# Optimization experiments

Measured on AMD Instinct MI355X. Metric: run time of the kernel, lower is better.

## Reference

```python
import jax, jax.numpy as jnp
import numpy as np

POOL = 7          # pool_size
RES = 42          # ROIS_resolution
CH = 2048         # backbone output channels (Xception)
GCN_DIM = 256     # gcn_outfeat_dim (== gat_outfeat_dim after head split, heads=1)
HEADS = 1
GAT_CH = 256
ALPHA = 0.1       # APPNP teleport
EPS = 1e-3        # keras BatchNormalization epsilon
CHUNKS = CH // GCN_DIM            # 8 channel chunks per ROI
CNODES = CHUNKS * POOL * POOL     # 392 intra-graph nodes


def _rois():
    # fixed ROI boxes (x, y, w, h) on the 42x42 upsampled map:
    # 3x3 grid of 14x14 cells + two horizontal halves + full image
    c = RES // 3
    r = [(x * c, y * c, c, c) for y in range(3) for x in range(3)]
    r += [(0, 0, RES, RES // 2), (0, RES // 2, RES, RES // 2), (0, 0, RES, RES)]
    return r

ROIS = _rois()
NUM_ROIS = len(ROIS)  # 12


def _gcn_adj(n):
    # spektral GCNConv.preprocess on all-ones adjacency: D^-1/2 (A + I) D^-1/2
    a = np.ones((n, n), np.float32) + np.eye(n, dtype=np.float32)
    d = a.sum(1)
    return jnp.asarray(a / np.sqrt(np.outer(d, d)))

A_INTRA = _gcn_adj(CNODES)        # (392, 392)
A_INTER = _gcn_adj(NUM_ROIS + 1)  # (13, 13)


def _appnp(x, a, w, b):
    # APPNPConv, propagations=1, sigmoid MLP: (1-a)*A@m + a*m
    m = jax.nn.sigmoid(x @ w + b)
    return (1.0 - ALPHA) * jnp.einsum('nm,...mf->...nf', a, m) + ALPHA * m


def _gat(x, a, k, a_self, a_neigh, b):
    # GATConv._call_dense (inference: dropout off); a has add_self_loops folded in
    xp = jnp.einsum('...ni,iho->...nho', x, k)          # (...,N,H,C)
    s = jnp.einsum('...nhi,iho->...nho', xp, a_self)    # (...,N,H,1)
    t = jnp.einsum('...nhi,iho->...nho', xp, a_neigh)   # (...,N,H,1)
    coef = s + jnp.swapaxes(t, -3, -1)                  # (...,N,H,N)
    coef = jax.nn.leaky_relu(coef, 0.2)
    mask = jnp.where(a == 0.0, -1e10, 0.0)              # (N,N) (all-connected here)
    coef = jax.nn.softmax(coef + mask[:, None, :], axis=-1)
    out = jnp.einsum('...nhm,...mhi->...nhi', coef, xp)
    out = out.reshape(out.shape[:-2] + (HEADS * GAT_CH,))  # concat heads
    return jax.nn.elu(out + b)


def _gnn_block(x, a, aw, ab, gk, gs, gn, gb):
    h = _appnp(x, a, aw, ab) + x
    return _gat(h, a, gk, gs, gn, gb) + h


def setup_inputs() -> dict:
    key = jax.random.key(0)
    ks = jax.random.split(key, 8)
    s = 0.05
    return {
        'base_out': jax.random.normal(ks[0], (8, POOL, POOL, CH), jnp.float32),
        'appnp_w': jax.random.normal(ks[1], (GCN_DIM, GCN_DIM), jnp.float32) * s,
        'appnp_b': jnp.zeros((GCN_DIM,), jnp.float32),
        'gat_kernel': jax.random.normal(ks[2], (GCN_DIM, HEADS, GAT_CH), jnp.float32) * s,
        'gat_attn_self': jax.random.normal(ks[3], (GAT_CH, HEADS, 1), jnp.float32) * s,
        'gat_attn_neighs': jax.random.normal(ks[4], (GAT_CH, HEADS, 1), jnp.float32) * s,
        'gat_bias': jnp.zeros((HEADS * GAT_CH,), jnp.float32),
        'pool_feat_w': jax.random.normal(ks[5], (GCN_DIM, 2 * GCN_DIM), jnp.float32) * s,
        'pool_feat_b': jnp.zeros((2 * GCN_DIM,), jnp.float32),
        'pool_attn_w': jax.random.normal(ks[6], (GCN_DIM, 2 * GCN_DIM), jnp.float32) * s,
        'pool_attn_b': jnp.zeros((2 * GCN_DIM,), jnp.float32),
        'bn_gamma': jnp.ones((2 * GCN_DIM,), jnp.float32),
        'bn_beta': jnp.zeros((2 * GCN_DIM,), jnp.float32),
        'bn_mean': jnp.zeros((2 * GCN_DIM,), jnp.float32),
        'bn_var': jnp.ones((2 * GCN_DIM,), jnp.float32),
        'dense_w': jax.random.normal(ks[7], (2 * GCN_DIM, 200), jnp.float32) * s,
        'dense_b': jnp.zeros((200,), jnp.float32),
    }


def reference(base_out, appnp_w, appnp_b, gat_kernel, gat_attn_self, gat_attn_neighs,
              gat_bias, pool_feat_w, pool_feat_b, pool_attn_w, pool_attn_b,
              bn_gamma, bn_beta, bn_mean, bn_var, dense_w, dense_b):
    B = base_out.shape[0]
    # upsample backbone features to ROI resolution
    x0 = jax.image.resize(base_out, (B, RES, RES, CH), 'bilinear')
    # RoiPoolingConv: crop each static ROI and resize to (POOL, POOL)
    pooled = [jax.image.resize(x0[:, y:y + h, x:x + w, :], (B, POOL, POOL, CH), 'bilinear')
              for (x, y, w, h) in ROIS]
    pooled.append(base_out)  # global node (pool_size == base_out spatial dim)
    rois = jnp.stack(pooled, axis=1)  # (B, R+1, 7, 7, CH)
    # _temp_nodes_transform: split channels into CHUNKS, concat along node axis
    nodes = rois.reshape(B, NUM_ROIS + 1, POOL * POOL, CHUNKS, GCN_DIM)
    nodes = nodes.transpose(0, 1, 3, 2, 4).reshape(B, NUM_ROIS + 1, CNODES, GCN_DIM)
    gnn = (appnp_w, appnp_b, gat_kernel, gat_attn_self, gat_attn_neighs, gat_bias)
    # intra-ROI graphs: 13 independent 392-node graphs (batched over (B, R+1))
    x2_intra = _gnn_block(nodes, A_INTRA, *gnn).reshape(B, (NUM_ROIS + 1) * CNODES, GCN_DIM)
    # inter-ROI graphs: 392 independent 13-node graphs
    xt = nodes.transpose(0, 2, 1, 3)  # (B, CNODES, R+1, GCN_DIM)
    x2_inter = _gnn_block(xt, A_INTER, *gnn).reshape(B, CNODES * (NUM_ROIS + 1), GCN_DIM)
    x2 = jnp.concatenate([x2_intra, x2_inter], axis=1)  # (B, 10192, 256)
    # GlobalAttentionPool(512)
    feat = x2 @ pool_feat_w + pool_feat_b
    gate = jax.nn.sigmoid(x2 @ pool_attn_w + pool_attn_b)
    xf = jnp.sum(gate * feat, axis=1)  # (B, 512)
    # BatchNorm (inference) + softmax classifier
    xn = (xf - bn_mean) / jnp.sqrt(bn_var + EPS) * bn_gamma + bn_beta
    return jax.nn.softmax(xn @ dense_w + dense_b, axis=-1)
```

## Files before the change

### kernel.cpp

```cpp
#include <hip/hip_runtime.h>
#include <math.h>


typedef __attribute__((ext_vector_type(8))) short bf16x8;
typedef __attribute__((ext_vector_type(4))) float f32x4;
typedef __attribute__((ext_vector_type(4))) short short4v;

#define MFMA16x32(a, b, c) __builtin_amdgcn_mfma_f32_16x16x32_bf16((a), (b), (c), 0, 0, 0)

__device__ __forceinline__ float sigmoidf_(float x) { return 1.0f / (1.0f + expf(-x)); }
__device__ __forceinline__ float leakyf_(float x) { return x >= 0.0f ? x : 0.2f * x; }
__device__ __forceinline__ float eluf_(float x) { return x > 0.0f ? x : expm1f(x); }
__device__ __forceinline__ short f2bf(float f) {
  unsigned u = __builtin_bit_cast(unsigned, f);
  unsigned r = u + 0x7fffu + ((u >> 16) & 1u);
  return (short)(r >> 16);
}
__device__ __forceinline__ float bf2f(short s) {
  unsigned u = ((unsigned)(unsigned short)s) << 16;
  return __builtin_bit_cast(float, u);
}
__device__ __forceinline__ f32x4 fzero4() {
  f32x4 z;
  #pragma unroll
  for (int i = 0; i < 4; ++i) z[i] = 0.0f;
  return z;
}

__global__ void wtab_k(float* __restrict__ wtab) {
  const int RX[12] = {0,14,28, 0,14,28, 0,14,28, 0, 0, 0};
  const int RY[12] = {0, 0, 0,14,14,14,28,28,28, 0,21, 0};
  const int RW[12] = {14,14,14,14,14,14,14,14,14,42,42,42};
  const int RH[12] = {14,14,14,14,14,14,14,14,14,21,21,42};
  for (int e = threadIdx.x; e < 13 * 2 * 49; e += blockDim.x) {
    const int roi = e / 98;
    const int rest = e % 98;
    const int axis = rest / 49;
    const int o = (rest % 49) / 7;
    const int ib = rest % 7;
    float wout;
    if (roi == 12) {
      wout = (o == ib) ? 1.0f : 0.0f;
    } else {
      const int start = axis ? RX[roi] : RY[roi];
      const int len = axis ? RW[roi] : RH[roi];
      const float s = (float)len / 7.0f;
      const float oc = (o + 0.5f) * s - 0.5f;
      float wsum = 0.0f, dot = 0.0f;
      for (int j = 0; j < len; ++j) {
        float w = 1.0f - fabsf((float)j - oc) / s;
        if (w <= 0.0f) continue;
        wsum += w;
        const float ic = ((float)(start + j) + 0.5f) / 6.0f - 0.5f;
        const float fl = floorf(ic);
        const int ia = (int)fl;
        const float fr = ic - fl;
        int c0 = ia;     if (c0 < 0) c0 = 0; if (c0 > 6) c0 = 6;
        int c1 = ia + 1; if (c1 < 0) c1 = 0; if (c1 > 6) c1 = 6;
        float u = 0.0f;
        if (c0 == ib) u += 1.0f - fr;
        if (c1 == ib) u += fr;
        dot += w * u;
      }
      wout = dot / wsum;
    }
    wtab[e] = wout;
  }
}

__global__ void wcvt_k(const float* __restrict__ src, short* __restrict__ hi,
                       int K, int N) {
  const int idx = blockIdx.x * 256 + threadIdx.x;
  if (idx >= K * N) return;
  const int k = idx / N, n = idx % N;
  hi[(size_t)n * K + k] = f2bf(src[idx]);
}

__global__ void wcvt_pool_k(const float* __restrict__ Wf, const float* __restrict__ Wa,
                            short* __restrict__ BT) {
  const int idx = blockIdx.x * 256 + threadIdx.x;
  if (idx >= 1024 * 256) return;
  const int n = idx >> 8, k = idx & 255;
  const int p = n >> 4, i = n & 15;
  const int sc = ((p >> 1) << 4) + i;
  const float v = (p & 1) ? Wa[(size_t)k * 512 + sc] : Wf[(size_t)k * 512 + sc];
  BT[(size_t)n * 256 + k] = f2bf(v);
}

__global__ void wvec_k(const float* __restrict__ Wk, const float* __restrict__ as,
                       const float* __restrict__ an, float* __restrict__ was,
                       float* __restrict__ wan) {
  const int w = threadIdx.x >> 6, l = threadIdx.x & 63;
  const int row = blockIdx.x * 4 + w;
  const float* p = Wk + (size_t)row * 256;
  float s = 0.0f, t = 0.0f;
  #pragma unroll
  for (int j = 0; j < 4; ++j) {
    const int o = l + j * 64;
    const float v = p[o];
    s = fmaf(v, as[o], s);
    t = fmaf(v, an[o], t);
  }
  #pragma unroll
  for (int off = 32; off; off >>= 1) { s += __shfl_down(s, off); t += __shfl_down(t, off); }
  if (l == 0) { was[row] = s; wan[row] = t; }
}

__global__ __launch_bounds__(256) void nodes_k(const float* __restrict__ base,
                                               const float* __restrict__ wtab,
                                               short* __restrict__ nodes) {
  const int blk = blockIdx.x;
  const int chunk = blk & 7;
  const int br = blk >> 3;
  const int r = br % 13;
  const int b = br / 13;
  const int f = threadIdx.x;
  __shared__ float W49[49][50];
  const float* wv = wtab + (r * 2 + 0) * 49;
  const float* wh = wtab + (r * 2 + 1) * 49;
  for (int e = f; e < 2401; e += 256) {
    const int o = e / 49, in = e % 49;
    W49[o][in] = wv[(o / 7) * 7 + in / 7] * wh[(o % 7) * 7 + in % 7];
  }
  __syncthreads();
  float bv[49];
  const float* bp = base + (size_t)b * 49 * 2048 + chunk * 256 + f;
  #pragma unroll
  for (int in = 0; in < 49; ++in) bv[in] = bp[(size_t)in * 2048];
  const size_t obase = ((size_t)(b * 13 + r) * 392 + chunk * 49) * 256 + f;
  for (int o = 0; o < 49; ++o) {
    float acc = 0.0f;
    #pragma unroll
    for (int in = 0; in < 49; ++in) acc = fmaf(W49[o][in], bv[in], acc);
    nodes[obase + (size_t)o * 256] = f2bf(acc);
  }
}

enum { EP_PLAIN = 0, EP_SIG = 1, EP_PV = 2, EP_POOL = 3 };

template <int EPI>
__global__ __launch_bounds__(256) void gemm_t(
    const short* __restrict__ A, const short* __restrict__ BT,
    const int Kpad, const int nkt, const int Mvalid,
    const float* __restrict__ e0, const float* __restrict__ e1,
    const short* __restrict__ e2, short* __restrict__ Cs,
    float* __restrict__ xf) {
  const int tid = threadIdx.x;
  const int w = tid >> 6, l = tid & 63;
  const int lr = l & 15, kb = l >> 4;
  const int wr = w >> 1, wc = w & 1;

  int row0, col0, g = 0, rbase = 0, bseg = 0;
  const short* Ap;
  const short* Bp;
  if constexpr (EPI == EP_POOL) {
    const int bid = blockIdx.x;
    const int eff = (bid & 7) * 640 + (bid >> 3);
    const int mt = eff >> 3, ct = eff & 7;
    row0 = mt * 128; col0 = ct * 128;
    rbase = (mt % 40) * 128;
    bseg = (mt / 40) & 7;
    Ap = A; Bp = BT;
  } else if constexpr (EPI == EP_PV) {
    g = blockIdx.z;
    row0 = blockIdx.x * 128; col0 = blockIdx.y * 128;
    Ap = A + (size_t)g * 512 * 448;
    Bp = BT + (size_t)g * 256 * 448;
  } else {
    row0 = blockIdx.x * 128; col0 = blockIdx.y * 128;
    Ap = A; Bp = BT;
  }

  __shared__ short As[128][32];
  __shared__ short Bs[128][32];

  const int srow = w * 32 + (l >> 2);
  const int sso = (l & 3) * 8;
  const short* ag0 = Ap + (size_t)(row0 + srow) * Kpad + sso;
  const short* ag1 = ag0 + (size_t)16 * Kpad;
  const short* bg0 = Bp + (size_t)(col0 + srow) * Kpad + sso;
  const short* bg1 = bg0 + (size_t)16 * Kpad;

  f32x4 acc[4][4];
  #pragma unroll
  for (int i = 0; i < 4; ++i)
    #pragma unroll
    for (int j = 0; j < 4; ++j) acc[i][j] = fzero4();

  bf16x8 ra0 = *(const bf16x8*)ag0;
  bf16x8 ra1 = *(const bf16x8*)ag1;
  bf16x8 rb0 = *(const bf16x8*)bg0;
  bf16x8 rb1 = *(const bf16x8*)bg1;

  for (int kt = 0; kt < nkt; ++kt) {
    __syncthreads();
    *(bf16x8*)&As[srow][sso] = ra0;
    *(bf16x8*)&As[srow + 16][sso] = ra1;
    *(bf16x8*)&Bs[srow][sso] = rb0;
    *(bf16x8*)&Bs[srow + 16][sso] = rb1;
    if (kt + 1 < nkt) {
      const int ko = (kt + 1) * 32;
      ra0 = *(const bf16x8*)(ag0 + ko);
      ra1 = *(const bf16x8*)(ag1 + ko);
      rb0 = *(const bf16x8*)(bg0 + ko);
      rb1 = *(const bf16x8*)(bg1 + ko);
    }
    __syncthreads();
    bf16x8 va[4], vb[4];
    #pragma unroll
    for (int i = 0; i < 4; ++i) va[i] = *(const bf16x8*)&As[wr * 64 + i * 16 + lr][kb * 8];
    #pragma unroll
    for (int j = 0; j < 4; ++j) vb[j] = *(const bf16x8*)&Bs[wc * 64 + j * 16 + lr][kb * 8];
    #pragma unroll
    for (int i = 0; i < 4; ++i)
      #pragma unroll
      for (int j = 0; j < 4; ++j) acc[i][j] = MFMA16x32(va[i], vb[j], acc[i][j]);
  }

  if constexpr (EPI == EP_PLAIN || EPI == EP_SIG) {
    #pragma unroll
    for (int j = 0; j < 4; ++j) {
      const int col = col0 + wc * 64 + j * 16 + lr;
      float bs = 0.0f;
      if constexpr (EPI == EP_SIG) bs = e0[col];
      #pragma unroll
      for (int i = 0; i < 4; ++i) {
        const int row = row0 + wr * 64 + i * 16 + kb * 4;
        #pragma unroll
        for (int r = 0; r < 4; ++r) {
          if (row + r < Mvalid) {
            float o = acc[i][j][r];
            if constexpr (EPI == EP_SIG) o = sigmoidf_(o + bs);
            Cs[(size_t)(row + r) * 256 + col] = f2bf(o);
          }
        }
      }
    }
  } else if constexpr (EPI == EP_PV) {
    const int bb = g / 13, rr = g % 13;
    #pragma unroll
    for (int j = 0; j < 4; ++j) {
      const int col = col0 + wc * 64 + j * 16 + lr;
      const float bv = e1[col];
      #pragma unroll
      for (int i = 0; i < 4; ++i) {
        const int rl = row0 + wr * 64 + i * 16 + kb * 4;
        #pragma unroll
        for (int r = 0; r < 4; ++r) {
          const int row = rl + r;
          if (row < 392) {
            const size_t grow = (size_t)g * 392 + row;
            const float o = acc[i][j][r] * e0[grow];
            const float val = eluf_(o + bv) + bf2f(e2[grow * 256 + col]);
            Cs[((size_t)bb * 5120 + rr * 392 + row) * 256 + col] = f2bf(val);
          }
        }
      }
    }
  } else {
    #pragma unroll
    for (int jp = 0; jp < 2; ++jp) {
      const int j = jp * 2;
      const int cg = col0 + wc * 64 + j * 16;
      const int realcol = ((cg >> 5) << 4) + lr;
      const float bfv = e0[realcol], bav = e1[realcol];
      float cs = 0.0f;
      #pragma unroll
      for (int i = 0; i < 4; ++i) {
        const int rl = rbase + wr * 64 + i * 16 + kb * 4;
        #pragma unroll
        for (int r = 0; r < 4; ++r) {
          if (rl + r < 5096) {
            const float fv = acc[i][j][r] + bfv;
            const float gv = acc[i][j + 1][r] + bav;
            cs += sigmoidf_(gv) * fv;
          }
        }
      }
      cs += __shfl_xor(cs, 16);
      cs += __shfl_xor(cs, 32);
      if (l < 16) atomicAdd(&xf[(size_t)bseg * 512 + realcol], cs);
    }
  }
}

__global__ __launch_bounds__(256) void transpose_k(const short* __restrict__ xp,
                                                   short* __restrict__ xpT) {
  const int m0 = blockIdx.x * 64;
  const int f0 = blockIdx.y * 64;
  const int g = blockIdx.z;
  const int tid = threadIdx.x;
  __shared__ short tile[64][66];
  const int c = tid & 63;
  const int r4 = tid >> 6;
  #pragma unroll
  for (int p = 0; p < 16; ++p) {
    const int row = p * 4 + r4;
    const int m = m0 + row;
    tile[row][c] = (m < 392) ? xp[((size_t)g * 392 + m) * 256 + f0 + c] : (short)0;
  }
  __syncthreads();
  #pragma unroll
  for (int p = 0; p < 16; ++p) {
    const int fr = p * 4 + r4;
    xpT[((size_t)g * 256 + f0 + fr) * 448 + m0 + c] = tile[c][fr];
  }
}

__global__ void sums_intra_k(const short* __restrict__ m, float* __restrict__ S) {
  const int g = blockIdx.x;
  const int f = threadIdx.x;
  const short* p = m + (size_t)g * 392 * 256 + f;
  float a0 = 0.0f, a1 = 0.0f, a2 = 0.0f, a3 = 0.0f;
  for (int c = 0; c < 392; c += 4) {
    a0 += bf2f(p[(size_t)(c + 0) * 256]);
    a1 += bf2f(p[(size_t)(c + 1) * 256]);
    a2 += bf2f(p[(size_t)(c + 2) * 256]);
    a3 += bf2f(p[(size_t)(c + 3) * 256]);
  }
  S[(size_t)g * 256 + f] = (a0 + a1) + (a2 + a3);
}

__global__ void sums_inter_k(const short* __restrict__ m, float* __restrict__ S) {
  const int g = blockIdx.x;
  const int b = g / 392, c = g % 392;
  const int f = threadIdx.x;
  const short* p = m + ((size_t)(b * 13) * 392 + c) * 256 + f;
  float acc = 0.0f;
  #pragma unroll
  for (int r = 0; r < 13; ++r) acc += bf2f(p[(size_t)r * 392 * 256]);
  S[(size_t)g * 256 + f] = acc;
}

__global__ void h_intra_v(const short* __restrict__ nodes, const short* __restrict__ m,
                          const float* __restrict__ S, short* __restrict__ h) {
  const size_t e0 = ((size_t)blockIdx.x * 256 + threadIdx.x) * 8;
  const int row = (int)(e0 >> 8);
  const int f0 = (int)(e0 & 255);
  const int g = row / 392;
  const bf16x8 mv8 = *(const bf16x8*)(m + e0);
  const bf16x8 nv8 = *(const bf16x8*)(nodes + e0);
  const float* Sp = S + (size_t)g * 256 + f0;
  bf16x8 o;
  #pragma unroll
  for (int i = 0; i < 8; ++i) {
    const float mv = bf2f(mv8[i]);
    o[i] = f2bf(0.9f * (Sp[i] + mv) * (1.0f / 393.0f) + 0.1f * mv + bf2f(nv8[i]));
  }
  *(bf16x8*)(h + e0) = o;
}

__global__ void h_inter_v(const short* __restrict__ nodes, const short* __restrict__ m,
                          const float* __restrict__ S, short* __restrict__ h) {
  const size_t e0 = ((size_t)blockIdx.x * 256 + threadIdx.x) * 8;
  const int row = (int)(e0 >> 8);
  const int f0 = (int)(e0 & 255);
  const int b = row / 5096;
  const int c = row % 392;
  const int g = b * 392 + c;
  const bf16x8 mv8 = *(const bf16x8*)(m + e0);
  const bf16x8 nv8 = *(const bf16x8*)(nodes + e0);
  const float* Sp = S + (size_t)g * 256 + f0;
  bf16x8 o;
  #pragma unroll
  for (int i = 0; i < 8; ++i) {
    const float mv = bf2f(mv8[i]);
    o[i] = f2bf(0.9f * (Sp[i] + mv) * (1.0f / 14.0f) + 0.1f * mv + bf2f(nv8[i]));
  }
  *(bf16x8*)(h + e0) = o;
}

__global__ void st_h_k(const short* __restrict__ h, const float* __restrict__ was,
                       const float* __restrict__ wan, float* __restrict__ sb,
                       float* __restrict__ tb, int M) {
  const int row = (int)(((size_t)blockIdx.x * blockDim.x + threadIdx.x) >> 6);
  const int lane = threadIdx.x & 63;
  if (row >= M) return;
  const short4v v = *(const short4v*)(h + (size_t)row * 256 + lane * 4);
  float s = 0.0f, t = 0.0f;
  #pragma unroll
  for (int j = 0; j < 4; ++j) {
    const float x = bf2f(v[j]);
    s = fmaf(x, was[lane * 4 + j], s);
    t = fmaf(x, wan[lane * 4 + j], t);
  }
  #pragma unroll
  for (int off = 32; off; off >>= 1) { s += __shfl_down(s, off); t += __shfl_down(t, off); }
  if (lane == 0) { sb[row] = s; tb[row] = t; }
}

__global__ __launch_bounds__(256) void attn_e_k(const float* __restrict__ sb,
    const float* __restrict__ tb, short* __restrict__ E, float* __restrict__ dinv) {
  const int g = blockIdx.y;
  const int n0 = blockIdx.x * 32;
  const int tid = threadIdx.x;
  __shared__ float t_s[392];
  __shared__ float red[256];
  for (int i = tid; i < 392; i += 256) t_s[i] = tb[(size_t)g * 392 + i];
  __syncthreads();
  float lm = -1e30f;
  for (int i = tid; i < 392; i += 256) lm = fmaxf(lm, t_s[i]);
  red[tid] = lm;
  __syncthreads();
  for (int off = 128; off; off >>= 1) {
    if (tid < off) red[tid] = fmaxf(red[tid], red[tid + off]);
    __syncthreads();
  }
  const float tmax = red[0];
  const int n = n0 + (tid >> 3);
  const int ml = tid & 7;
  const bool nv = (n < 392);
  const float sv = nv ? sb[(size_t)g * 392 + n] : 0.0f;
  const float lt = leakyf_(sv + tmax);
  float d = 0.0f;
  short* erow = E + ((size_t)g * 512 + n) * 448;
  for (int c = 0; c < 7; ++c) {
    const int mb = c * 64 + ml * 8;
    bf16x8 ev;
    #pragma unroll
    for (int i = 0; i < 8; ++i) {
      const int m = mb + i;
      float e = 0.0f;
      if (nv && m < 392) { e = expf(leakyf_(sv + t_s[m]) - lt); d += e; }
      ev[i] = f2bf(e);
    }
    *(bf16x8*)(erow + mb) = ev;
  }
  d += __shfl_xor(d, 1); d += __shfl_xor(d, 2); d += __shfl_xor(d, 4);
  if (nv && ml == 0) dinv[(size_t)g * 392 + n] = 1.0f / d;
}

__global__ __launch_bounds__(256) void attn_inter_k(const short* __restrict__ xp,
    const float* __restrict__ sb, const float* __restrict__ tb,
    const short* __restrict__ h, const float* __restrict__ bias,
    short* __restrict__ x2, int B) {
  const int g = blockIdx.x;
  const int b = g / 392, c = g % 392;
  const int tid = threadIdx.x;
  __shared__ float xps[13][256];
  __shared__ float e_s[13][14];
  __shared__ float sv[13], tv[13], denom[13];
  __shared__ float tmax_s;
  for (int lin = tid; lin < 13 * 256; lin += 256) {
    const int r = lin >> 8, f = lin & 255;
    xps[r][f] = bf2f(xp[((size_t)(b * 13 + r) * 392 + c) * 256 + f]);
  }
  if (tid < 13) {
    const size_t row = (size_t)(b * 13 + tid) * 392 + c;
    sv[tid] = sb[row];
    tv[tid] = tb[row];
  }
  __syncthreads();
  if (tid == 0) {
    float mx = tv[0];
    for (int r = 1; r < 13; ++r) mx = fmaxf(mx, tv[r]);
    tmax_s = mx;
  }
  __syncthreads();
  if (tid < 169) {
    const int n = tid / 13, mm = tid % 13;
    e_s[n][mm] = expf(leakyf_(sv[n] + tv[mm]) - leakyf_(sv[n] + tmax_s));
  }
  __syncthreads();
  if (tid < 13) {
    float d = 0.0f;
    for (int mm = 0; mm < 13; ++mm) d += e_s[tid][mm];
    denom[tid] = d;
  }
  __syncthreads();
  const int f = tid;
  for (int n = 0; n < 13; ++n) {
    float acc = 0.0f;
    #pragma unroll
    for (int mm = 0; mm < 13; ++mm) acc = fmaf(e_s[n][mm], xps[mm][f], acc);
    const float o = acc / denom[n];
    const size_t hbase = ((size_t)(b * 13 + n) * 392 + c) * 256 + f;
    x2[(((size_t)(B + b)) * 5120 + (size_t)n * 392 + c) * 256 + f] =
        f2bf(eluf_(o + bias[f]) + bf2f(h[hbase]));
  }
}

__global__ __launch_bounds__(256) void head_k(const float* __restrict__ xf,
    const float* __restrict__ gamma, const float* __restrict__ beta,
    const float* __restrict__ mean, const float* __restrict__ var,
    const float* __restrict__ Wd, const float* __restrict__ bd,
    float* __restrict__ out) {
  const int b = blockIdx.x;
  const int tid = threadIdx.x;
  __shared__ float xn[512];
  __shared__ float red[256];
  for (int i = tid; i < 512; i += 256) {
    const float v = xf[(size_t)b * 512 + i];
    xn[i] = (v - mean[i]) / sqrtf(var[i] + 1e-3f) * gamma[i] + beta[i];
  }
  __syncthreads();
  float logit = -1e30f;
  if (tid < 200) {
    float acc = bd[tid];
    for (int i = 0; i < 512; ++i) acc = fmaf(xn[i], Wd[(size_t)i * 200 + tid], acc);
    logit = acc;
  }
  red[tid] = logit;
  __syncthreads();
  for (int off = 128; off; off >>= 1) {
    if (tid < off) red[tid] = fmaxf(red[tid], red[tid + off]);
    __syncthreads();
  }
  const float mx = red[0];
  __syncthreads();
  const float e = (tid < 200) ? expf(logit - mx) : 0.0f;
  red[tid] = e;
  __syncthreads();
  for (int off = 128; off; off >>= 1) {
    if (tid < off) red[tid] += red[tid + off];
    __syncthreads();
  }
  const float inv = 1.0f / red[0];
  if (tid < 200) out[(size_t)b * 200 + tid] = e * inv;
}

extern "C" void kernel_launch(void* const* d_in, const int* in_sizes, int n_in,
                              void* d_out, int out_size, void* d_ws, size_t ws_size,
                              hipStream_t stream) {
  (void)n_in; (void)out_size; (void)ws_size;
  const float* base    = (const float*)d_in[0];
  const float* appnp_w = (const float*)d_in[1];
  const float* appnp_b = (const float*)d_in[2];
  const float* gat_k   = (const float*)d_in[3];
  const float* gat_as  = (const float*)d_in[4];
  const float* gat_an  = (const float*)d_in[5];
  const float* gat_b   = (const float*)d_in[6];
  const float* pf_w    = (const float*)d_in[7];
  const float* pf_b    = (const float*)d_in[8];
  const float* pa_w    = (const float*)d_in[9];
  const float* pa_b    = (const float*)d_in[10];
  const float* bn_g    = (const float*)d_in[11];
  const float* bn_be   = (const float*)d_in[12];
  const float* bn_mu   = (const float*)d_in[13];
  const float* bn_va   = (const float*)d_in[14];
  const float* dw      = (const float*)d_in[15];
  const float* db      = (const float*)d_in[16];
  float* out = (float*)d_out;

  const int B = in_sizes[0] / (49 * 2048);
  const int G = B * 13;
  const int R = G * 392;
  const int Mt = (R + 127) / 128;
  const int Rpad = Mt * 128;
  const int MP = 2 * B * 5120;

  char* ws = (char*)d_ws;
  size_t off = 0;
  auto alloc = [&](size_t bytes) -> void* {
    void* p = (void*)(ws + off);
    off += (bytes + 255) & ~(size_t)255;
    return p;
  };
  float* wtab   = (float*)alloc((size_t)13 * 2 * 49 * 4);
  short* aWhi   = (short*)alloc((size_t)256 * 256 * 2);
  short* gkhi   = (short*)alloc((size_t)256 * 256 * 2);
  short* pwcomb = (short*)alloc((size_t)1024 * 256 * 2);
  float* was    = (float*)alloc((size_t)256 * 4);
  float* wan    = (float*)alloc((size_t)256 * 4);
  short* nodes  = (short*)alloc((size_t)Rpad * 256 * 2);
  short* mbuf   = (short*)alloc((size_t)R * 256 * 2);
  short* hbuf   = (short*)alloc((size_t)Rpad * 256 * 2);
  short* xpbuf  = (short*)alloc((size_t)R * 256 * 2);
  short* xpT    = (short*)alloc((size_t)G * 256 * 448 * 2);
  short* Ebuf   = (short*)alloc((size_t)G * 512 * 448 * 2);
  short* x2buf  = (short*)alloc((size_t)MP * 256 * 2);
  float* Sintra = (float*)alloc((size_t)G * 256 * 4);
  float* Sinter = (float*)alloc((size_t)B * 392 * 256 * 4);
  float* sbuf   = (float*)alloc((size_t)R * 4);
  float* tbuf   = (float*)alloc((size_t)R * 4);
  float* dinv   = (float*)alloc((size_t)R * 4);
  float* xf     = (float*)alloc((size_t)B * 512 * 4);

  hipMemsetAsync(xf, 0, (size_t)B * 512 * 4, stream);
  wtab_k<<<1, 256, 0, stream>>>(wtab);
  wcvt_k<<<(256 * 256 + 255) / 256, 256, 0, stream>>>(appnp_w, aWhi, 256, 256);
  wcvt_k<<<(256 * 256 + 255) / 256, 256, 0, stream>>>(gat_k, gkhi, 256, 256);
  wcvt_pool_k<<<1024, 256, 0, stream>>>(pf_w, pa_w, pwcomb);
  wvec_k<<<64, 256, 0, stream>>>(gat_k, gat_as, gat_an, was, wan);
  nodes_k<<<B * 13 * 8, 256, 0, stream>>>(base, wtab, nodes);

  gemm_t<EP_SIG><<<dim3(Mt, 2), 256, 0, stream>>>(nodes, aWhi, 256, 8, R,
      appnp_b, nullptr, nullptr, mbuf, nullptr);
  sums_intra_k<<<G, 256, 0, stream>>>(mbuf, Sintra);
  sums_inter_k<<<B * 392, 256, 0, stream>>>(mbuf, Sinter);

  h_intra_v<<<R / 8, 256, 0, stream>>>(nodes, mbuf, Sintra, hbuf);
  gemm_t<EP_PLAIN><<<dim3(Mt, 2), 256, 0, stream>>>(hbuf, gkhi, 256, 8, R,
      nullptr, nullptr, nullptr, xpbuf, nullptr);
  st_h_k<<<R / 4, 256, 0, stream>>>(hbuf, was, wan, sbuf, tbuf, R);
  transpose_k<<<dim3(7, 4, G), 256, 0, stream>>>(xpbuf, xpT);
  attn_e_k<<<dim3(14, G), 256, 0, stream>>>(sbuf, tbuf, Ebuf, dinv);
  gemm_t<EP_PV><<<dim3(4, 2, G), 256, 0, stream>>>(Ebuf, xpT, 448, 14, 392,
      dinv, gat_b, hbuf, x2buf, nullptr);

  h_inter_v<<<R / 8, 256, 0, stream>>>(nodes, mbuf, Sinter, hbuf);
  gemm_t<EP_PLAIN><<<dim3(Mt, 2), 256, 0, stream>>>(hbuf, gkhi, 256, 8, R,
      nullptr, nullptr, nullptr, xpbuf, nullptr);
  st_h_k<<<R / 4, 256, 0, stream>>>(hbuf, was, wan, sbuf, tbuf, R);
  attn_inter_k<<<B * 392, 256, 0, stream>>>(xpbuf, sbuf, tbuf, hbuf, gat_b, x2buf, B);

  gemm_t<EP_POOL><<<5120, 256, 0, stream>>>(x2buf, pwcomb, 256, 8, 0,
      pf_b, pa_b, nullptr, nullptr, xf);
  head_k<<<B, 256, 0, stream>>>(xf, bn_g, bn_be, bn_mu, bn_va, dw, db, out);
}
```

Measured before the change: 432.0 us.

## Fuse GAT attention-score generation into PV GEMM and merge h/st kernels

The intra-graph GAT no longer materialises the bf16 attention matrix E in global memory. A new flash-style kernel recomputes exp(leaky(s+t)-max) on the fly into shared memory and feeds it straight to MFMA, while a separate denom_k kernel computes the softmax denominators. The h-update kernels now also compute the attention dot products s and t, which removes the st_h_k launches and a re-read of h. The cost is redundant exp work across column tiles and fewer blocks in the PV grid (2x2xG versus 4x2xG), which lowers parallelism.

Result: faster. 418.3 us (-3.2%).

```diff
diff --git a/kernel.cpp b/kernel.cpp
--- a/kernel.cpp
+++ b/kernel.cpp
@@ -4,7 +4,6 @@
 
 typedef __attribute__((ext_vector_type(8))) short bf16x8;
 typedef __attribute__((ext_vector_type(4))) float f32x4;
-typedef __attribute__((ext_vector_type(4))) short short4v;
 
 #define MFMA16x32(a, b, c) __builtin_amdgcn_mfma_f32_16x16x32_bf16((a), (b), (c), 0, 0, 0)
 
@@ -136,23 +135,20 @@
   }
 }
 
-enum { EP_PLAIN = 0, EP_SIG = 1, EP_PV = 2, EP_POOL = 3 };
+enum { EP_PLAIN = 0, EP_SIG = 1, EP_POOL = 3 };
 
 template <int EPI>
 __global__ __launch_bounds__(256) void gemm_t(
     const short* __restrict__ A, const short* __restrict__ BT,
     const int Kpad, const int nkt, const int Mvalid,
     const float* __restrict__ e0, const float* __restrict__ e1,
-    const short* __restrict__ e2, short* __restrict__ Cs,
-    float* __restrict__ xf) {
+    short* __restrict__ Cs, float* __restrict__ xf) {
   const int tid = threadIdx.x;
   const int w = tid >> 6, l = tid & 63;
   const int lr = l & 15, kb = l >> 4;
   const int wr = w >> 1, wc = w & 1;
 
-  int row0, col0, g = 0, rbase = 0, bseg = 0;
-  const short* Ap;
-  const short* Bp;
+  int row0, col0, rbase = 0, bseg = 0;
   if constexpr (EPI == EP_POOL) {
     const int bid = blockIdx.x;
     const int eff = (bid & 7) * 640 + (bid >> 3);
@@ -160,15 +156,8 @@
     row0 = mt * 128; col0 = ct * 128;
     rbase = (mt % 40) * 128;
     bseg = (mt / 40) & 7;
-    Ap = A; Bp = BT;
-  } else if constexpr (EPI == EP_PV) {
-    g = blockIdx.z;
-    row0 = blockIdx.x * 128; col0 = blockIdx.y * 128;
-    Ap = A + (size_t)g * 512 * 448;
-    Bp = BT + (size_t)g * 256 * 448;
   } else {
     row0 = blockIdx.x * 128; col0 = blockIdx.y * 128;
-    Ap = A; Bp = BT;
   }
 
   __shared__ short As[128][32];
@@ -176,9 +165,9 @@
 
   const int srow = w * 32 + (l >> 2);
   const int sso = (l & 3) * 8;
-  const short* ag0 = Ap + (size_t)(row0 + srow) * Kpad + sso;
+  const short* ag0 = A + (size_t)(row0 + srow) * Kpad + sso;
   const short* ag1 = ag0 + (size_t)16 * Kpad;
-  const short* bg0 = Bp + (size_t)(col0 + srow) * Kpad + sso;
+  const short* bg0 = BT + (size_t)(col0 + srow) * Kpad + sso;
   const short* bg1 = bg0 + (size_t)16 * Kpad;
 
   f32x4 acc[4][4];
@@ -236,27 +225,6 @@
         }
       }
     }
-  } else if constexpr (EPI == EP_PV) {
-    const int bb = g / 13, rr = g % 13;
-    #pragma unroll
-    for (int j = 0; j < 4; ++j) {
-      const int col = col0 + wc * 64 + j * 16 + lr;
-      const float bv = e1[col];
-      #pragma unroll
-      for (int i = 0; i < 4; ++i) {
-        const int rl = row0 + wr * 64 + i * 16 + kb * 4;
-        #pragma unroll
-        for (int r = 0; r < 4; ++r) {
-          const int row = rl + r;
-          if (row < 392) {
-            const size_t grow = (size_t)g * 392 + row;
-            const float o = acc[i][j][r] * e0[grow];
-            const float val = eluf_(o + bv) + bf2f(e2[grow * 256 + col]);
-            Cs[((size_t)bb * 5120 + rr * 392 + row) * 256 + col] = f2bf(val);
-          }
-        }
-      }
-    }
   } else {
     #pragma unroll
     for (int jp = 0; jp < 2; ++jp) {
@@ -284,6 +252,145 @@
   }
 }
 
+__global__ __launch_bounds__(256) void pv_flash_k(
+    const short* __restrict__ xpT, const float* __restrict__ sb,
+    const float* __restrict__ tb, const float* __restrict__ dinv,
+    const float* __restrict__ bias, const short* __restrict__ h,
+    short* __restrict__ x2) {
+  const int g = blockIdx.z;
+  const int rh = blockIdx.y;
+  const int ct = blockIdx.x;
+  const int tid = threadIdx.x;
+  const int w = tid >> 6, l = tid & 63;
+  const int lr = l & 15, kb = l >> 4;
+  const int wr = w >> 1, wc = w & 1;
+
+  __shared__ short As[128][32];
+  __shared__ short Bs[128][32];
+  __shared__ float t_s[416];
+  __shared__ float red[256];
+
+  for (int i = tid; i < 416; i += 256)
+    t_s[i] = (i < 392) ? tb[(size_t)g * 392 + i] : -1e30f;
+  __syncthreads();
+  float lm = -1e30f;
+  for (int i = tid; i < 392; i += 256) lm = fmaxf(lm, t_s[i]);
+  red[tid] = lm;
+  __syncthreads();
+  for (int off = 128; off; off >>= 1) {
+    if (tid < off) red[tid] = fmaxf(red[tid], red[tid + off]);
+    __syncthreads();
+  }
+  const float tmax = red[0];
+
+  const int srow = w * 32 + (l >> 2);
+  const int sso = (l & 3) * 8;
+  const short* bg0 = xpT + ((size_t)g * 256 + ct * 128 + srow) * 448 + sso;
+  const short* bg1 = bg0 + (size_t)16 * 448;
+  const int bb = g / 13, rr = g % 13;
+
+  for (int rt = 0; rt < 2; ++rt) {
+    const int row0 = rh * 256 + rt * 128;
+    const int ar0 = row0 + srow, ar1 = row0 + srow + 16;
+    const bool v0 = ar0 < 392, v1 = ar1 < 392;
+    const float sv0 = v0 ? sb[(size_t)g * 392 + ar0] : 0.0f;
+    const float sv1 = v1 ? sb[(size_t)g * 392 + ar1] : 0.0f;
+    const float lt0 = leakyf_(sv0 + tmax);
+    const float lt1 = leakyf_(sv1 + tmax);
+
+    f32x4 acc[4][4];
+    #pragma unroll
+    for (int i = 0; i < 4; ++i)
+      #pragma unroll
+      for (int j = 0; j < 4; ++j) acc[i][j] = fzero4();
+
+    bf16x8 rb0 = *(const bf16x8*)bg0;
+    bf16x8 rb1 = *(const bf16x8*)bg1;
+
+    for (int kt = 0; kt < 13; ++kt) {
+      __syncthreads();
+      *(bf16x8*)&Bs[srow][sso] = rb0;
+      *(bf16x8*)&Bs[srow + 16][sso] = rb1;
+      {
+        const int mb = kt * 32 + sso;
+        bf16x8 e0v, e1v;
+        #pragma unroll
+        for (int i = 0; i < 8; ++i) {
+          const float tm = t_s[mb + i];
+          e0v[i] = v0 ? f2bf(__expf(leakyf_(sv0 + tm) - lt0)) : (short)0;
+          e1v[i] = v1 ? f2bf(__expf(leakyf_(sv1 + tm) - lt1)) : (short)0;
+        }
+        *(bf16x8*)&As[srow][sso] = e0v;
+        *(bf16x8*)&As[srow + 16][sso] = e1v;
+      }
+      if (kt + 1 < 13) {
+        const int ko = (kt + 1) * 32;
+        rb0 = *(const bf16x8*)(bg0 + ko);
+        rb1 = *(const bf16x8*)(bg1 + ko);
+      }
+      __syncthreads();
+      bf16x8 va[4], vb[4];
+      #pragma unroll
+      for (int i = 0; i < 4; ++i) va[i] = *(const bf16x8*)&As[wr * 64 + i * 16 + lr][kb * 8];
+      #pragma unroll
+      for (int j = 0; j < 4; ++j) vb[j] = *(const bf16x8*)&Bs[wc * 64 + j * 16 + lr][kb * 8];
+      #pragma unroll
+      for (int i = 0; i < 4; ++i)
+        #pragma unroll
+        for (int j = 0; j < 4; ++j) acc[i][j] = MFMA16x32(va[i], vb[j], acc[i][j]);
+    }
+
+    #pragma unroll
+    for (int j = 0; j < 4; ++j) {
+      const int col = ct * 128 + wc * 64 + j * 16 + lr;
+      const float bv = bias[col];
+      #pragma unroll
+      for (int i = 0; i < 4; ++i) {
+        const int rl = row0 + wr * 64 + i * 16 + kb * 4;
+        #pragma unroll
+        for (int r = 0; r < 4; ++r) {
+          const int row = rl + r;
+          if (row < 392) {
+            const size_t grow = (size_t)g * 392 + row;
+            const float o = acc[i][j][r] * dinv[grow];
+            const float val = eluf_(o + bv) + bf2f(h[grow * 256 + col]);
+            x2[((size_t)bb * 5120 + rr * 392 + row) * 256 + col] = f2bf(val);
+          }
+        }
+      }
+    }
+  }
+}
+
+__global__ __launch_bounds__(256) void denom_k(const float* __restrict__ sb,
+    const float* __restrict__ tb, float* __restrict__ dinv) {
+  const int g = blockIdx.x;
+  const int tid = threadIdx.x;
+  __shared__ float t_s[392];
+  __shared__ float red[256];
+  for (int i = tid; i < 392; i += 256) t_s[i] = tb[(size_t)g * 392 + i];
+  __syncthreads();
+  float lm = -1e30f;
+  for (int i = tid; i < 392; i += 256) lm = fmaxf(lm, t_s[i]);
+  red[tid] = lm;
+  __syncthreads();
+  for (int off = 128; off; off >>= 1) {
+    if (tid < off) red[tid] = fmaxf(red[tid], red[tid + off]);
+    __syncthreads();
+  }
+  const float tmax = red[0];
+  for (int n = tid; n < 392; n += 256) {
+    const float sv = sb[(size_t)g * 392 + n];
+    const float lt = leakyf_(sv + tmax);
+    float d0 = 0.0f, d1 = 0.0f;
+    for (int m = 0; m < 392; m += 2) {
+      d0 += __expf(leakyf_(sv + t_s[m]) - lt);
+      d1 += __expf(leakyf_(sv + t_s[m + 1]) - lt);
+    }
+    dinv[(size_t)g * 392 + n] = 1.0f / (d0 + d1);
+  }
+}
+
 __global__ __launch_bounds__(256) void transpose_k(const short* __restrict__ xp,
                                                    short* __restrict__ xpT) {
   const int m0 = blockIdx.x * 64;
@@ -332,102 +439,38 @@
   S[(size_t)g * 256 + f] = acc;
 }
 
-__global__ void h_intra_v(const short* __restrict__ nodes, const short* __restrict__ m,
-                          const float* __restrict__ S, short* __restrict__ h) {
-  const size_t e0 = ((size_t)blockIdx.x * 256 + threadIdx.x) * 8;
-  const int row = (int)(e0 >> 8);
-  const int f0 = (int)(e0 & 255);
-  const int g = row / 392;
+template <int INTRA>
+__global__ void h_st_v(const short* __restrict__ nodes, const short* __restrict__ m,
+                       const float* __restrict__ S, const float* __restrict__ was,
+                       const float* __restrict__ wan, short* __restrict__ h,
+                       float* __restrict__ sb, float* __restrict__ tb) {
+  const int row = blockIdx.x * 8 + (threadIdx.x >> 5);
+  const int f0 = (threadIdx.x & 31) * 8;
+  int g;
+  float inv;
+  if constexpr (INTRA) { g = row / 392; inv = 1.0f / 393.0f; }
+  else { const int b = row / 5096; g = b * 392 + row % 392; inv = 1.0f / 14.0f; }
+  const size_t e0 = (size_t)row * 256 + f0;
   const bf16x8 mv8 = *(const bf16x8*)(m + e0);
   const bf16x8 nv8 = *(const bf16x8*)(nodes + e0);
   const float* Sp = S + (size_t)g * 256 + f0;
   bf16x8 o;
+  float s = 0.0f, t = 0.0f;
   #pragma unroll
   for (int i = 0; i < 8; ++i) {
     const float mv = bf2f(mv8[i]);
-    o[i] = f2bf(0.9f * (Sp[i] + mv) * (1.0f / 393.0f) + 0.1f * mv + bf2f(nv8[i]));
+    const float hv = 0.9f * (Sp[i] + mv) * inv + 0.1f * mv + bf2f(nv8[i]);
+    o[i] = f2bf(hv);
+    s = fmaf(hv, was[f0 + i], s);
+    t = fmaf(hv, wan[f0 + i], t);
   }
   *(bf16x8*)(h + e0) = o;
-}
-
-__global__ void h_inter_v(const short* __restrict__ nodes, const short* __restrict__ m,
-                          const float* __restrict__ S, short* __restrict__ h) {
-  const size_t e0 = ((size_t)blockIdx.x * 256 + threadIdx.x) * 8;
-  const int row = (int)(e0 >> 8);
-  const int f0 = (int)(e0 & 255);
-  const int b = row / 5096;
-  const int c = row % 392;
-  const int g = b * 392 + c;
-  const bf16x8 mv8 = *(const bf16x8*)(m + e0);
-  const bf16x8 nv8 = *(const bf16x8*)(nodes + e0);
-  const float* Sp = S + (size_t)g * 256 + f0;
-  bf16x8 o;
-  #pragma unroll
-  for (int i = 0; i < 8; ++i) {
-    const float mv = bf2f(mv8[i]);
-    o[i] = f2bf(0.9f * (Sp[i] + mv) * (1.0f / 14.0f) + 0.1f * mv + bf2f(nv8[i]));
-  }
-  *(bf16x8*)(h + e0) = o;
-}
-
-__global__ void st_h_k(const short* __restrict__ h, const float* __restrict__ was,
-                       const float* __restrict__ wan, float* __restrict__ sb,
-                       float* __restrict__ tb, int M) {
-  const int row = (int)(((size_t)blockIdx.x * blockDim.x + threadIdx.x) >> 6);
-  const int lane = threadIdx.x & 63;
-  if (row >= M) return;
-  const short4v v = *(const short4v*)(h + (size_t)row * 256 + lane * 4);
-  float s = 0.0f, t = 0.0f;
-  #pragma unroll
-  for (int j = 0; j < 4; ++j) {
-    const float x = bf2f(v[j]);
-    s = fmaf(x, was[lane * 4 + j], s);
-    t = fmaf(x, wan[lane * 4 + j], t);
-  }
-  #pragma unroll
-  for (int off = 32; off; off >>= 1) { s += __shfl_down(s, off); t += __shfl_down(t, off); }
-  if (lane == 0) { sb[row] = s; tb[row] = t; }
-}
-
-__global__ __launch_bounds__(256) void attn_e_k(const float* __restrict__ sb,
-    const float* __restrict__ tb, short* __restrict__ E, float* __restrict__ dinv) {
-  const int g = blockIdx.y;
-  const int n0 = blockIdx.x * 32;
-  const int tid = threadIdx.x;
-  __shared__ float t_s[392];
-  __shared__ float red[256];
-  for (int i = tid; i < 392; i += 256) t_s[i] = tb[(size_t)g * 392 + i];
-  __syncthreads();
-  float lm = -1e30f;
-  for (int i = tid; i < 392; i += 256) lm = fmaxf(lm, t_s[i]);
-  red[tid] = lm;
-  __syncthreads();
-  for (int off = 128; off; off >>= 1) {
-    if (tid < off) red[tid] = fmaxf(red[tid], red[tid + off]);
-    __syncthreads();
-  }
-  const float tmax = red[0];
-  const int n = n0 + (tid >> 3);
-  const int ml = tid & 7;
-  const bool nv = (n < 392);
-  const float sv = nv ? sb[(size_t)g * 392 + n] : 0.0f;
-  const float lt = leakyf_(sv + tmax);
-  float d = 0.0f;
-  short* erow = E + ((size_t)g * 512 + n) * 448;
-  for (int c = 0; c < 7; ++c) {
-    const int mb = c * 64 + ml * 8;
-    bf16x8 ev;
-    #pragma unroll
-    for (int i = 0; i < 8; ++i) {
-      const int m = mb + i;
-      float e = 0.0f;
-      if (nv && m < 392) { e = expf(leakyf_(sv + t_s[m]) - lt); d += e; }
-      ev[i] = f2bf(e);
-    }
-    *(bf16x8*)(erow + mb) = ev;
-  }
-  d += __shfl_xor(d, 1); d += __shfl_xor(d, 2); d += __shfl_xor(d, 4);
-  if (nv && ml == 0) dinv[(size_t)g * 392 + n] = 1.0f / d;
+  #pragma unroll
+  for (int off = 16; off; off >>= 1) {
+    s += __shfl_xor(s, off, 32);
+    t += __shfl_xor(t, off, 32);
+  }
+  if ((threadIdx.x & 31) == 0) { sb[row] = s; tb[row] = t; }
 }
 
 __global__ __launch_bounds__(256) void attn_inter_k(const short* __restrict__ xp,
@@ -567,7 +610,6 @@
   short* hbuf   = (short*)alloc((size_t)Rpad * 256 * 2);
   short* xpbuf  = (short*)alloc((size_t)R * 256 * 2);
   short* xpT    = (short*)alloc((size_t)G * 256 * 448 * 2);
-  short* Ebuf   = (short*)alloc((size_t)G * 512 * 448 * 2);
   short* x2buf  = (short*)alloc((size_t)MP * 256 * 2);
   float* Sintra = (float*)alloc((size_t)G * 256 * 4);
   float* Sinter = (float*)alloc((size_t)B * 392 * 256 * 4);
@@ -585,26 +627,24 @@
   nodes_k<<<B * 13 * 8, 256, 0, stream>>>(base, wtab, nodes);
 
   gemm_t<EP_SIG><<<dim3(Mt, 2), 256, 0, stream>>>(nodes, aWhi, 256, 8, R,
-      appnp_b, nullptr, nullptr, mbuf, nullptr);
+      appnp_b, nullptr, mbuf, nullptr);
   sums_intra_k<<<G, 256, 0, stream>>>(mbuf, Sintra);
   sums_inter_k<<<B * 392, 256, 0, stream>>>(mbuf, Sinter);
 
-  h_intra_v<<<R / 8, 256, 0, stream>>>(nodes, mbuf, Sintra, hbuf);
+  h_st_v<1><<<R / 8, 256, 0, stream>>>(nodes, mbuf, Sintra, was, wan, hbuf, sbuf, tbuf);
   gemm_t<EP_PLAIN><<<dim3(Mt, 2), 256, 0, stream>>>(hbuf, gkhi, 256, 8, R,
-      nullptr, nullptr, nullptr, xpbuf, nullptr);
-  st_h_k<<<R / 4, 256, 0, stream>>>(hbuf, was, wan, sbuf, tbuf, R);
+      nullptr, nullptr, xpbuf, nullptr);
   transpose_k<<<dim3(7, 4, G), 256, 0, stream>>>(xpbuf, xpT);
-  attn_e_k<<<dim3(14, G), 256, 0, stream>>>(sbuf, tbuf, Ebuf, dinv);
-  gemm_t<EP_PV><<<dim3(4, 2, G), 256, 0, stream>>>(Ebuf, xpT, 448, 14, 392,
-      dinv, gat_b, hbuf, x2buf, nullptr);
-
-  h_inter_v<<<R / 8, 256, 0, stream>>>(nodes, mbuf, Sinter, hbuf);
+  denom_k<<<G, 256, 0, stream>>>(sbuf, tbuf, dinv);
+  pv_flash_k<<<dim3(2, 2, G), 256, 0, stream>>>(xpT, sbuf, tbuf, dinv, gat_b,
+                                                hbuf, x2buf);
+
+  h_st_v<0><<<R / 8, 256, 0, stream>>>(nodes, mbuf, Sinter, was, wan, hbuf, sbuf, tbuf);
   gemm_t<EP_PLAIN><<<dim3(Mt, 2), 256, 0, stream>>>(hbuf, gkhi, 256, 8, R,
-      nullptr, nullptr, nullptr, xpbuf, nullptr);
-  st_h_k<<<R / 4, 256, 0, stream>>>(hbuf, was, wan, sbuf, tbuf, R);
+      nullptr, nullptr, xpbuf, nullptr);
   attn_inter_k<<<B * 392, 256, 0, stream>>>(xpbuf, sbuf, tbuf, hbuf, gat_b, x2buf, B);
 
   gemm_t<EP_POOL><<<5120, 256, 0, stream>>>(x2buf, pwcomb, 256, 8, 0,
-      pf_b, pa_b, nullptr, nullptr, xf);
+      pf_b, pa_b, nullptr, xf);
   head_k<<<B, 256, 0, stream>>>(xf, bn_g, bn_be, bn_mu, bn_va, dw, db, out);
 }
```
